# Kernel tuning notes

Hardware: AMD Instinct MI355X
Metric: run time of the kernel (lower is better)

## Reference

```python
import jax, jax.numpy as jnp
import numpy as np
import math

HEADS = 4
KV = 960
CH = (64, 128, 256, 512)
B, H, W = 8, 32, 32
EPS_IN = 1e-5  # nn.InstanceNorm2d default eps


def conv2d(x, w, groups=1, pad=0):
    # x: [N,C,H,W], w: [O, C//groups, kh, kw]
    return jax.lax.conv_general_dilated(
        x, w, (1, 1), [(pad, pad), (pad, pad)],
        feature_group_count=groups,
        dimension_numbers=('NCHW', 'OIHW', 'NCHW'))


def l2norm(x):
    # torch F.normalize(dim=-1): x / max(||x||_2, 1e-12)
    return x / jnp.maximum(jnp.linalg.norm(x, axis=-1, keepdims=True), 1e-12)


def setup_inputs() -> dict:
    key = jax.random.key(0)
    ks = iter(jax.random.split(key, 40))
    s = 0.02
    d = {}
    for i, c in enumerate(CH, 1):
        d[f'emb{i}'] = jax.random.normal(next(ks), (B, c, H, W), jnp.float32)
    d['emb_all'] = jax.random.normal(next(ks), (B, KV, H, W), jnp.float32)
    for i, c in enumerate(CH, 1):
        d[f'Wm{i}'] = jax.random.normal(next(ks), (c * HEADS, c, 1, 1), jnp.float32) * s
        # grouped 3x3: groups = c*HEADS//2 -> 2 in-channels per group
        d[f'Wq{i}'] = jax.random.normal(next(ks), (c * HEADS, 2, 3, 3), jnp.float32) * s
        d[f'Wp{i}'] = jax.random.normal(next(ks), (c, c, 1, 1), jnp.float32) * s
    d['Wmk'] = jax.random.normal(next(ks), (KV * HEADS, KV, 1, 1), jnp.float32) * s
    d['Wmv'] = jax.random.normal(next(ks), (KV * HEADS, KV, 1, 1), jnp.float32) * s
    # depthwise 3x3: groups = KV*HEADS
    d['Wk'] = jax.random.normal(next(ks), (KV * HEADS, 1, 3, 3), jnp.float32) * s
    d['Wv'] = jax.random.normal(next(ks), (KV * HEADS, 1, 3, 3), jnp.float32) * s
    return d


def _forward(emb1, emb2, emb3, emb4, emb_all,
             Wm1, Wq1, Wp1, Wm2, Wq2, Wp2, Wm3, Wq3, Wp3, Wm4, Wq4, Wp4,
             Wmk, Wmv, Wk, Wv):
    b, _, h, w = emb1.shape
    hw = h * w
    # shared K/V: 1x1 multi-head expand then depthwise 3x3
    k = conv2d(conv2d(emb_all, Wmk), Wk, groups=KV * HEADS, pad=1)
    v = conv2d(conv2d(emb_all, Wmv), Wv, groups=KV * HEADS, pad=1)
    k = l2norm(k.reshape(b, HEADS, KV, hw))   # [b,H,KV,hw]
    v = v.reshape(b, HEADS, KV, hw)
    scale = 1.0 / math.sqrt(KV)
    outs = []
    for emb, Wm, Wq, Wp in ((emb1, Wm1, Wq1, Wp1), (emb2, Wm2, Wq2, Wp2),
                            (emb3, Wm3, Wq3, Wp3), (emb4, Wm4, Wq4, Wp4)):
        c = emb.shape[1]
        q = conv2d(conv2d(emb, Wm), Wq, groups=c * HEADS // 2, pad=1)
        q = l2norm(q.reshape(b, HEADS, c, hw))            # [b,H,c,hw]
        attn = jnp.einsum('bhcn,bhdn->bhcd', q, k) * scale  # [b,H,c,KV]
        # InstanceNorm2d over (c, KV) per (b, head), no affine, biased var
        mu = attn.mean(axis=(2, 3), keepdims=True)
        var = attn.var(axis=(2, 3), keepdims=True)
        probs = jax.nn.softmax((attn - mu) / jnp.sqrt(var + EPS_IN), axis=-1)
        # dropout rate 0 (inference) -> identity
        out = jnp.einsum('bhcd,bhdn->bhcn', probs, v).mean(axis=1)  # head-mean -> [b,c,hw]
        outs.append(conv2d(out.reshape(b, c, h, w), Wp))
    return tuple(outs)


def reference(emb1, emb2, emb3, emb4, emb_all,
              Wm1, Wq1, Wp1, Wm2, Wq2, Wp2, Wm3, Wq3, Wp3, Wm4, Wq4, Wp4,
              Wmk, Wmv, Wk, Wv):
    return _forward(emb1, emb2, emb3, emb4, emb_all,
                    Wm1, Wq1, Wp1, Wm2, Wq2, Wp2, Wm3, Wq3, Wp3, Wm4, Wq4, Wp4,
                    Wmk, Wmv, Wk, Wv)
```

## Files before the change

kernel.cpp:

```cpp
#include <hip/hip_runtime.h>
#include <hip/hip_bf16.h>
#include <math.h>

typedef __hip_bfloat16 bf16;
typedef __attribute__((ext_vector_type(8))) short short8;
typedef __attribute__((ext_vector_type(8))) unsigned short u16x8;
typedef __attribute__((ext_vector_type(4))) float f32x4;
typedef long long ll;

#define B_ 8
#define HEADS_ 4
#define KV_ 960
#define HW_ 1024
#define CKV_ 3840

__device__ __forceinline__ float wredsum(float v) {
#pragma unroll
  for (int o = 32; o > 0; o >>= 1) v += __shfl_xor(v, o);
  return v;
}
__device__ __forceinline__ float wredmax(float v) {
#pragma unroll
  for (int o = 32; o > 0; o >>= 1) v = fmaxf(v, __shfl_xor(v, o));
  return v;
}

__device__ __forceinline__ float bfu2f(unsigned short u) {
  union { unsigned int i; float f; } c;
  c.i = ((unsigned int)u) << 16;
  return c.f;
}
__device__ __forceinline__ unsigned short f2bfu(float f) {
  bf16 h = __float2bfloat16(f);
  return *(unsigned short*)&h;
}

__device__ __forceinline__ void gl_lds16(const void* g, void* l) {
  __builtin_amdgcn_global_load_lds(
      (const __attribute__((address_space(1))) unsigned*)g,
      (__attribute__((address_space(3))) unsigned*)l, 16, 0, 0);
}

__global__ void __launch_bounds__(256) castw(const float* __restrict__ in,
                                             bf16* __restrict__ out, int n) {
  int i = (blockIdx.x * 256 + threadIdx.x) * 4;
  if (i < n) {
    float4 v = *(const float4*)(in + i);
    out[i] = __float2bfloat16(v.x);
    out[i + 1] = __float2bfloat16(v.y);
    out[i + 2] = __float2bfloat16(v.z);
    out[i + 3] = __float2bfloat16(v.w);
  }
}

template <typename InT>
__global__ void __launch_bounds__(256) tcast(const InT* __restrict__ in,
                                             bf16* __restrict__ out, int R,
                                             ll inZ, ll outZ) {
  __shared__ float t[32][33];
  const int x = threadIdx.x & 31, y0 = threadIdx.x >> 5;
  const int c0 = blockIdx.x << 5, r0 = blockIdx.y << 5;
  const InT* ip = in + (ll)blockIdx.z * inZ + (ll)r0 * 1024 + c0;
  bf16* op = out + (ll)blockIdx.z * outZ + (ll)c0 * R + r0;
#pragma unroll
  for (int i = 0; i < 4; i++) {
    int r = y0 + i * 8;
    float v;
    if constexpr (__is_same(InT, float)) v = ip[(ll)r * 1024 + x];
    else v = __bfloat162float(ip[(ll)r * 1024 + x]);
    t[r][x] = v;
  }
  __syncthreads();
#pragma unroll
  for (int i = 0; i < 4; i++) {
    int cc = y0 + i * 8;
    op[(ll)cc * R + x] = __float2bfloat16(t[x][cc]);
  }
}

template <int OUTMODE, bool STATS>
__global__ void __launch_bounds__(256) gemm_mfma(
    const bf16* __restrict__ A, const bf16* __restrict__ Bt, void* __restrict__ Y,
    int M, int N, int K, int nh,
    ll aZ, ll aH, ll bZ, ll bH, ll yZ, int ldy, float scale,
    float* __restrict__ part) {
  __shared__ bf16 As[2][128 * 32];
  __shared__ bf16 Bs[2][128 * 32];
  __shared__ float rs1[4], rs2[4];
  const int tid = threadIdx.x;
  const int lane = tid & 63;
  const int wave = tid >> 6;
  const int wr = wave >> 1, wc = wave & 1;

  const int gy = gridDim.y, gz = gridDim.z;
  int orig = (blockIdx.z * gy + blockIdx.y) * 8 + blockIdx.x;
  int cpx = (gy * gz);
  int flat = (orig & 7) * cpx + (orig >> 3);
  const int lx = flat & 7;
  int rest = flat >> 3;
  const int ly = rest % gy;
  const int lz = rest / gy;

  const int z = lz;
  const int m0 = ly << 7, n0 = lx << 7;

  f32x4 acc[4][4];
#pragma unroll
  for (int i = 0; i < 4; i++)
#pragma unroll
    for (int j = 0; j < 4; j++) acc[i][j] = (f32x4){0.f, 0.f, 0.f, 0.f};

  const int frow = lane & 15;
  const int kq = lane >> 4;

  const bf16* Ah = A + (ll)z * aZ;
  const bf16* Bh = Bt + (ll)z * bZ;
  int k0n = 0;

  auto stage = [&](int buf) {
#pragma unroll
    for (int t = 0; t < 2; t++) {
      const int e = (wave * 2 + t) * 64 + lane;
      const int row = e >> 2;
      const int ks = (e & 3) ^ ((row >> 1) & 3);
      int gr = m0 + row; gr = gr < M ? gr : M - 1;
      gl_lds16(Ah + (ll)gr * K + k0n + ks * 8,
               (char*)&As[buf][0] + (wave * 2 + t) * 1024);
      int rn = n0 + row; rn = rn < N ? rn : N - 1;
      gl_lds16(Bh + (ll)rn * K + k0n + ks * 8,
               (char*)&Bs[buf][0] + (wave * 2 + t) * 1024);
    }
  };

  const int kpt = K >> 5;
  const int iters = nh * kpt;
  stage(0);
  __syncthreads();

  int buf = 0;
  for (int it = 0; it < iters; ++it) {
    if (it + 1 < iters) {
      k0n += 32;
      if (k0n == K) { k0n = 0; Ah += aH; Bh += bH; }
      stage(buf ^ 1);
    }
    short8 af[4], bfr[4];
#pragma unroll
    for (int fm = 0; fm < 4; fm++) {
      const int row = wr * 64 + fm * 16 + frow;
      af[fm] = *(const short8*)&As[buf][((row << 2) | (kq ^ ((row >> 1) & 3))) << 3];
    }
#pragma unroll
    for (int fn = 0; fn < 4; fn++) {
      const int row = wc * 64 + fn * 16 + frow;
      bfr[fn] = *(const short8*)&Bs[buf][((row << 2) | (kq ^ ((row >> 1) & 3))) << 3];
    }
#pragma unroll
    for (int fm = 0; fm < 4; fm++)
#pragma unroll
      for (int fn = 0; fn < 4; fn++)
        acc[fm][fn] = __builtin_amdgcn_mfma_f32_16x16x32_bf16(
            af[fm], bfr[fn], acc[fm][fn], 0, 0, 0);
    __syncthreads();
    buf ^= 1;
  }

  const int rq = kq << 2;
  float lsum = 0.f, lsq = 0.f;
#pragma unroll
  for (int fm = 0; fm < 4; fm++) {
    const int mrow = m0 + wr * 64 + fm * 16 + rq;
#pragma unroll
    for (int fn = 0; fn < 4; fn++) {
      const int ncol = n0 + wc * 64 + fn * 16 + frow;
      if (ncol >= N) continue;
      if constexpr (OUTMODE == 0) {
        float* Yp = (float*)Y + (ll)z * yZ;
#pragma unroll
        for (int i = 0; i < 4; i++)
          if (mrow + i < M) {
            float v = acc[fm][fn][i] * scale;
            Yp[(ll)(mrow + i) * ldy + ncol] = v;
            if constexpr (STATS) { lsum += v; lsq += v * v; }
          }
      } else if constexpr (OUTMODE == 1) {
        bf16* Yp = (bf16*)Y + (ll)z * yZ;
#pragma unroll
        for (int i = 0; i < 4; i++)
          if (mrow + i < M)
            Yp[(ll)(mrow + i) * ldy + ncol] =
                __float2bfloat16(acc[fm][fn][i] * scale);
      } else {
        if (mrow < M) {
          bf16* Yp = (bf16*)Y + (ll)z * yZ + (ll)ncol * ldy + mrow;
#pragma unroll
          for (int i = 0; i < 4; i++)
            Yp[i] = __float2bfloat16(acc[fm][fn][i] * scale);
        }
      }
    }
  }
  if constexpr (STATS) {
    lsum = wredsum(lsum);
    lsq = wredsum(lsq);
    if (lane == 0) { rs1[wave] = lsum; rs2[wave] = lsq; }
    __syncthreads();
    if (tid == 0) {
      int slot = ly * 8 + lx;
      part[((ll)z * 32 + slot) * 2] = rs1[0] + rs1[1] + rs1[2] + rs1[3];
      part[((ll)z * 32 + slot) * 2 + 1] = rs2[0] + rs2[1] + rs2[2] + rs2[3];
    }
  }
}

template <int OUTMODE, bool STATS>
__global__ void __launch_bounds__(512, 2) gemm8(
    const bf16* __restrict__ A, const bf16* __restrict__ Bt, void* __restrict__ Y,
    int M, int N, int K, int nh,
    ll aZ, ll aH, ll bZ, ll bH, ll yZ, int ldy, float scale,
    float* __restrict__ part) {
  __shared__ char lds[131072];
  __shared__ float rs1[8], rs2[8];
  const int tid = threadIdx.x;
  const int lane = tid & 63;
  const int wave = tid >> 6;
  const int wm = wave >> 2, wn = wave & 3;

  const int nx = gridDim.x, my = gridDim.y;
  const int nwg = nx * my * gridDim.z;
  int orig = (blockIdx.z * my + blockIdx.y) * nx + blockIdx.x;
  int q8 = nwg >> 3, r8 = nwg & 7;
  int xcd = orig & 7, bidx = orig >> 3;
  int flat = (xcd < r8) ? xcd * (q8 + 1) + bidx
                        : r8 * (q8 + 1) + (xcd - r8) * q8 + bidx;
  const int lx = flat % nx;
  int rest = flat / nx;
  const int ly = rest % my;
  const int lz = rest / my;

  const int m0 = ly << 8, n0 = lx << 8;
  const int ktiles = K >> 6;
  const int nt = nh * ktiles;

  f32x4 acc[8][4];
#pragma unroll
  for (int i = 0; i < 8; i++)
#pragma unroll
    for (int j = 0; j < 4; j++) acc[i][j] = (f32x4){0.f, 0.f, 0.f, 0.f};

  const int frow = lane & 15;
  const int kq = lane >> 4;
  const int swz = frow & 7;

  auto stageRound = [&](int matB, int r, int tt, int buf) {
    int h = tt / ktiles;
    int koff = (tt % ktiles) << 6;
    int s = (r << 9) + tid;
    int row = s >> 3;
    int ks = (s & 7) ^ (row & 7);
    const bf16* src;
    char* dst;
    if (!matB) {
      int gr = m0 + row; gr = gr < M ? gr : M - 1;
      src = A + (ll)lz * aZ + (ll)h * aH + (ll)gr * K + koff + (ks << 3);
      dst = lds + buf * 32768 + (((r << 3) + wave) << 10);
    } else {
      int gr = n0 + row; gr = gr < N ? gr : N - 1;
      src = Bt + (ll)lz * bZ + (ll)h * bH + (ll)gr * K + koff + (ks << 3);
      dst = lds + 65536 + buf * 32768 + (((r << 3) + wave) << 10);
    }
    gl_lds16(src, dst);
  };

  auto readA = [&](int fm, int kh, int cur) -> short8 {
    int row = wm * 128 + fm * 16 + frow;
    int slot = (kq + (kh << 2)) ^ swz;
    return *(const short8*)(lds + cur * 32768 + row * 128 + slot * 16);
  };
  auto readB = [&](int fn, int kh, int cur) -> short8 {
    int row = wn * 64 + fn * 16 + frow;
    int slot = (kq + (kh << 2)) ^ swz;
    return *(const short8*)(lds + 65536 + cur * 32768 + row * 128 + slot * 16);
  };

  stageRound(1, 0, 0, 0); stageRound(1, 1, 0, 0);
  stageRound(1, 2, 0, 0); stageRound(1, 3, 0, 0);
  stageRound(0, 0, 0, 0); stageRound(0, 2, 0, 0);
  stageRound(0, 1, 0, 0); stageRound(0, 3, 0, 0);

  int cur = 0;
  for (int tt = 0; tt < nt; ++tt) {
    const bool hasNext = (tt + 1 < nt);
    short8 bfr[4][2];
#pragma unroll
    for (int p = 0; p < 4; p++) {
      if (p == 0) {
        if (hasNext) asm volatile("s_waitcnt vmcnt(2)" ::: "memory");
        else         asm volatile("s_waitcnt vmcnt(0)" ::: "memory");
        __builtin_amdgcn_s_barrier();
        __builtin_amdgcn_sched_barrier(0);
#pragma unroll
        for (int fn = 0; fn < 4; fn++)
#pragma unroll
          for (int kh = 0; kh < 2; kh++) bfr[fn][kh] = readB(fn, kh, cur);
      }
      if (p == 2) {
        if (hasNext) asm volatile("s_waitcnt vmcnt(6)" ::: "memory");
        __builtin_amdgcn_s_barrier();
        __builtin_amdgcn_sched_barrier(0);
      }
      short8 a0k0 = readA(2 * p, 0, cur), a0k1 = readA(2 * p, 1, cur);
      short8 a1k0 = readA(2 * p + 1, 0, cur), a1k1 = readA(2 * p + 1, 1, cur);
      if (hasNext) {
        if (p == 0) {
          stageRound(1, 0, tt + 1, cur ^ 1); stageRound(1, 1, tt + 1, cur ^ 1);
          stageRound(1, 2, tt + 1, cur ^ 1); stageRound(1, 3, tt + 1, cur ^ 1);
        } else if (p == 1) {
          stageRound(0, 0, tt + 1, cur ^ 1); stageRound(0, 2, tt + 1, cur ^ 1);
        } else if (p == 2) {
          stageRound(0, 1, tt + 1, cur ^ 1); stageRound(0, 3, tt + 1, cur ^ 1);
        }
      }
      __builtin_amdgcn_s_setprio(1);
#pragma unroll
      for (int fn = 0; fn < 4; fn++) {
        acc[2 * p][fn] = __builtin_amdgcn_mfma_f32_16x16x32_bf16(
            a0k0, bfr[fn][0], acc[2 * p][fn], 0, 0, 0);
        acc[2 * p][fn] = __builtin_amdgcn_mfma_f32_16x16x32_bf16(
            a0k1, bfr[fn][1], acc[2 * p][fn], 0, 0, 0);
        acc[2 * p + 1][fn] = __builtin_amdgcn_mfma_f32_16x16x32_bf16(
            a1k0, bfr[fn][0], acc[2 * p + 1][fn], 0, 0, 0);
        acc[2 * p + 1][fn] = __builtin_amdgcn_mfma_f32_16x16x32_bf16(
            a1k1, bfr[fn][1], acc[2 * p + 1][fn], 0, 0, 0);
      }
      __builtin_amdgcn_s_setprio(0);
    }
    cur ^= 1;
  }

  const int rq = kq << 2;
  float lsum = 0.f, lsq = 0.f;
#pragma unroll
  for (int fm = 0; fm < 8; fm++) {
    const int mrow = m0 + wm * 128 + fm * 16 + rq;
#pragma unroll
    for (int fn = 0; fn < 4; fn++) {
      const int ncol = n0 + wn * 64 + fn * 16 + frow;
      if (ncol >= N) continue;
      if constexpr (OUTMODE == 0) {
        float* Yp = (float*)Y + (ll)lz * yZ;
#pragma unroll
        for (int i = 0; i < 4; i++)
          if (mrow + i < M) {
            float v = acc[fm][fn][i] * scale;
            Yp[(ll)(mrow + i) * ldy + ncol] = v;
            if constexpr (STATS) { lsum += v; lsq += v * v; }
          }
      } else if constexpr (OUTMODE == 1) {
        bf16* Yp = (bf16*)Y + (ll)lz * yZ;
#pragma unroll
        for (int i = 0; i < 4; i++)
          if (mrow + i < M)
            Yp[(ll)(mrow + i) * ldy + ncol] =
                __float2bfloat16(acc[fm][fn][i] * scale);
      } else {
        if (mrow < M) {
          bf16* Yp = (bf16*)Y + (ll)lz * yZ + (ll)ncol * ldy + mrow;
#pragma unroll
          for (int i = 0; i < 4; i++)
            Yp[i] = __float2bfloat16(acc[fm][fn][i] * scale);
        }
      }
    }
  }
  if constexpr (STATS) {
    lsum = wredsum(lsum);
    lsq = wredsum(lsq);
    if (lane == 0) { rs1[wave] = lsum; rs2[wave] = lsq; }
    __syncthreads();
    if (tid == 0) {
      float s = 0.f, s2 = 0.f;
#pragma unroll
      for (int w = 0; w < 8; w++) { s += rs1[w]; s2 += rs2[w]; }
      int slot = ly * nx + lx;
      part[((ll)lz * 32 + slot) * 2] = s;
      part[((ll)lz * 32 + slot) * 2 + 1] = s2;
    }
  }
}

__global__ void __launch_bounds__(256) pv_reduce(const bf16* __restrict__ part,
                                                 bf16* __restrict__ out,
                                                 int planeShift) {
  const ll idx = ((ll)blockIdx.x * 256 + threadIdx.x) * 4;
  const int b = (int)(idx >> planeShift);
  const ll off = idx - ((ll)b << planeShift);
  const bf16* base = part + (((ll)b * 4) << planeShift) + off;
  float a0 = 0.f, a1 = 0.f, a2 = 0.f, a3 = 0.f;
#pragma unroll
  for (int s = 0; s < 4; s++) {
    ushort4 u = *(const ushort4*)(base + ((ll)s << planeShift));
    a0 += bfu2f(u.x); a1 += bfu2f(u.y); a2 += bfu2f(u.z); a3 += bfu2f(u.w);
  }
  ushort4 o;
  o.x = f2bfu(a0 * 0.25f);
  o.y = f2bfu(a1 * 0.25f);
  o.z = f2bfu(a2 * 0.25f);
  o.w = f2bfu(a3 * 0.25f);
  *(ushort4*)(out + idx) = o;
}

template <bool NORM>
__global__ void __launch_bounds__(256) dw3x3v(const bf16* __restrict__ in,
                                              const float* __restrict__ w9,
                                              bf16* __restrict__ out, int C) {
  __shared__ float tile[34][36];
  __shared__ float red[4];
  const int bc = blockIdx.x;
  const int ch = bc % C;
  const int tid = threadIdx.x;
  const int y = tid >> 3;
  const int x0 = (tid & 7) << 2;
  const bf16* ip = in + ((size_t)bc << 10);

  ushort4 u = *(const ushort4*)(ip + (y << 5) + x0);
  tile[y + 1][x0 + 1] = bfu2f(u.x);
  tile[y + 1][x0 + 2] = bfu2f(u.y);
  tile[y + 1][x0 + 3] = bfu2f(u.z);
  tile[y + 1][x0 + 4] = bfu2f(u.w);
  if (tid < 34) { tile[0][tid] = 0.f; tile[33][tid] = 0.f; }
  if (tid < 32) { tile[tid + 1][0] = 0.f; tile[tid + 1][33] = 0.f; }
  __syncthreads();

  const float* wc = w9 + ch * 9;
  float s[4] = {0.f, 0.f, 0.f, 0.f};
#pragma unroll
  for (int dy = 0; dy < 3; dy++) {
    const float* tr = &tile[y + dy][x0];
    float c0 = tr[0], c1 = tr[1], c2 = tr[2], c3 = tr[3], c4 = tr[4], c5 = tr[5];
    float wa = wc[dy * 3], wb = wc[dy * 3 + 1], wd = wc[dy * 3 + 2];
    s[0] += c0 * wa + c1 * wb + c2 * wd;
    s[1] += c1 * wa + c2 * wb + c3 * wd;
    s[2] += c2 * wa + c3 * wb + c4 * wd;
    s[3] += c3 * wa + c4 * wb + c5 * wd;
  }

  float inv = 1.f;
  if (NORM) {
    float ss = s[0] * s[0] + s[1] * s[1] + s[2] * s[2] + s[3] * s[3];
    ss = wredsum(ss);
    const int lane = tid & 63, wid = tid >> 6;
    if (lane == 0) red[wid] = ss;
    __syncthreads();
    inv = 1.0f / fmaxf(sqrtf(red[0] + red[1] + red[2] + red[3]), 1e-12f);
  }
  ushort4 o4;
  o4.x = f2bfu(s[0] * inv);
  o4.y = f2bfu(s[1] * inv);
  o4.z = f2bfu(s[2] * inv);
  o4.w = f2bfu(s[3] * inv);
  *(ushort4*)(out + ((size_t)bc << 10) + (y << 5) + x0) = o4;
}

__global__ void __launch_bounds__(256) dwtcast(const bf16* __restrict__ in,
                                               const float* __restrict__ w9,
                                               bf16* __restrict__ out) {
  __shared__ float t[3][32][34];
  const int jt = blockIdx.x;
  const int y = blockIdx.y;
  const int bh = blockIdx.z;
  const int b = bh >> 2, h = bh & 3;
  const int j0 = jt << 5;
  const int tid = threadIdx.x;

  if (tid < 192) {
    const int rr = tid / 64;
    const int rem = tid - rr * 64;
    const int jc = rem >> 1;
    const int half = rem & 1;
    const int iy = y - 1 + rr;
    float* dstp = &t[rr][jc][1 + (half << 4)];
    if (iy < 0 || iy > 31) {
#pragma unroll
      for (int u = 0; u < 16; u++) dstp[u] = 0.f;
    } else {
      const bf16* src = in + (((ll)b * CKV_ + h * KV_ + j0 + jc) << 10) +
                        (iy << 5) + (half << 4);
      u16x8 v0 = *(const u16x8*)src;
      u16x8 v1 = *(const u16x8*)(src + 8);
#pragma unroll
      for (int u = 0; u < 8; u++) dstp[u] = bfu2f(v0[u]);
#pragma unroll
      for (int u = 0; u < 8; u++) dstp[8 + u] = bfu2f(v1[u]);
    }
  }
  if (tid < 96) {
    const int rr = tid / 32, jc = tid - rr * 32;
    t[rr][jc][0] = 0.f;
    t[rr][jc][33] = 0.f;
  }
  __syncthreads();

  const int jp = tid & 15;
  const int xq = tid >> 4;
  const int ch0 = jp << 1;
  const float* wA = w9 + ((size_t)h * KV_ + j0 + ch0) * 9;
  const float* wB = wA + 9;

  bf16* orow = out + (ll)bh * 983040 + (ll)j0 + (ch0);
#pragma unroll
  for (int sx = 0; sx < 2; sx++) {
    const int x = xq + (sx << 4);
    float sA = 0.f, sB = 0.f;
#pragma unroll
    for (int dy = 0; dy < 3; dy++) {
      const float* rA = &t[dy][ch0][x];
      const float* rB = &t[dy][ch0 + 1][x];
      sA += rA[0] * wA[dy * 3] + rA[1] * wA[dy * 3 + 1] + rA[2] * wA[dy * 3 + 2];
      sB += rB[0] * wB[dy * 3] + rB[1] * wB[dy * 3 + 1] + rB[2] * wB[dy * 3 + 2];
    }
    const int n = (y << 5) + x;
    ushort2 o;
    o.x = f2bfu(sA);
    o.y = f2bfu(sB);
    *(ushort2*)(orow + (ll)n * 960) = o;
  }
}

__global__ void __launch_bounds__(256) gq3x3v(const bf16* __restrict__ in,
                                              const float* __restrict__ wq,
                                              bf16* __restrict__ out, int C4) {
  __shared__ float t0[34][36];
  __shared__ float t1[34][36];
  __shared__ float red[4];
  const int bo = blockIdx.x;
  const int o = bo % C4;
  const int b = bo / C4;
  const int ic0 = (o >> 1) << 1;
  const int tid = threadIdx.x;
  const int y = tid >> 3;
  const int x0 = (tid & 7) << 2;
  const bf16* p0 = in + (((size_t)b * C4 + ic0) << 10);

  ushort4 u0 = *(const ushort4*)(p0 + (y << 5) + x0);
  ushort4 u1 = *(const ushort4*)(p0 + 1024 + (y << 5) + x0);
  t0[y + 1][x0 + 1] = bfu2f(u0.x);
  t0[y + 1][x0 + 2] = bfu2f(u0.y);
  t0[y + 1][x0 + 3] = bfu2f(u0.z);
  t0[y + 1][x0 + 4] = bfu2f(u0.w);
  t1[y + 1][x0 + 1] = bfu2f(u1.x);
  t1[y + 1][x0 + 2] = bfu2f(u1.y);
  t1[y + 1][x0 + 3] = bfu2f(u1.z);
  t1[y + 1][x0 + 4] = bfu2f(u1.w);
  if (tid < 34) {
    t0[0][tid] = 0.f; t0[33][tid] = 0.f;
    t1[0][tid] = 0.f; t1[33][tid] = 0.f;
  }
  if (tid < 32) {
    t0[tid + 1][0] = 0.f; t0[tid + 1][33] = 0.f;
    t1[tid + 1][0] = 0.f; t1[tid + 1][33] = 0.f;
  }
  __syncthreads();

  const float* w = wq + o * 18;
  float s[4] = {0.f, 0.f, 0.f, 0.f};
#pragma unroll
  for (int dy = 0; dy < 3; dy++) {
    {
      const float* tr = &t0[y + dy][x0];
      float c0 = tr[0], c1 = tr[1], c2 = tr[2], c3 = tr[3], c4 = tr[4], c5 = tr[5];
      float wa = w[dy * 3], wb = w[dy * 3 + 1], wd = w[dy * 3 + 2];
      s[0] += c0 * wa + c1 * wb + c2 * wd;
      s[1] += c1 * wa + c2 * wb + c3 * wd;
      s[2] += c2 * wa + c3 * wb + c4 * wd;
      s[3] += c3 * wa + c4 * wb + c5 * wd;
    }
    {
      const float* tr = &t1[y + dy][x0];
      float c0 = tr[0], c1 = tr[1], c2 = tr[2], c3 = tr[3], c4 = tr[4], c5 = tr[5];
      float wa = w[9 + dy * 3], wb = w[9 + dy * 3 + 1], wd = w[9 + dy * 3 + 2];
      s[0] += c0 * wa + c1 * wb + c2 * wd;
      s[1] += c1 * wa + c2 * wb + c3 * wd;
      s[2] += c2 * wa + c3 * wb + c4 * wd;
      s[3] += c3 * wa + c4 * wb + c5 * wd;
    }
  }

  float ss = s[0] * s[0] + s[1] * s[1] + s[2] * s[2] + s[3] * s[3];
  ss = wredsum(ss);
  const int lane = tid & 63, wid = tid >> 6;
  if (lane == 0) red[wid] = ss;
  __syncthreads();
  float inv = 1.0f / fmaxf(sqrtf(red[0] + red[1] + red[2] + red[3]), 1e-12f);

  ushort4 o4;
  o4.x = f2bfu(s[0] * inv);
  o4.y = f2bfu(s[1] * inv);
  o4.z = f2bfu(s[2] * inv);
  o4.w = f2bfu(s[3] * inv);
  *(ushort4*)(out + ((size_t)bo << 10) + (y << 5) + x0) = o4;
}

__global__ void __launch_bounds__(256) softmax_rows(const float* __restrict__ attn,
                                                    const float* __restrict__ part,
                                                    int nslots,
                                                    bf16* __restrict__ probs, int c) {
  __shared__ float rm[4], rs[4];
  const int row = blockIdx.x;
  const int bh = row / c;
  const float* p = attn + (size_t)row * 960;
  bf16* op = probs + (size_t)row * 960;
  const int tid = threadIdx.x;

  float s = 0.f, s2 = 0.f;
  for (int i = 0; i < nslots; i++) {
    s += part[((ll)bh * 32 + i) * 2];
    s2 += part[((ll)bh * 32 + i) * 2 + 1];
  }
  const float n = (float)(c * 960);
  const float mu = s / n;
  const float var = s2 / n - mu * mu;
  const float rstd = rsqrtf(var + 1e-5f);

  float v[4];
  float mx = -1e30f;
#pragma unroll
  for (int u = 0; u < 4; u++) {
    int j = tid + (u << 8);
    if (j < 960) {
      v[u] = (p[j] - mu) * rstd;
      mx = fmaxf(mx, v[u]);
    } else {
      v[u] = -1e30f;
    }
  }
  mx = wredmax(mx);
  const int lane = tid & 63, wid = tid >> 6;
  if (lane == 0) rm[wid] = mx;
  __syncthreads();
  mx = fmaxf(fmaxf(rm[0], rm[1]), fmaxf(rm[2], rm[3]));

  float sum = 0.f;
#pragma unroll
  for (int u = 0; u < 4; u++) {
    int j = tid + (u << 8);
    if (j < 960) {
      v[u] = __expf(v[u] - mx);
      sum += v[u];
    }
  }
  sum = wredsum(sum);
  if (lane == 0) rs[wid] = sum;
  __syncthreads();
  sum = rs[0] + rs[1] + rs[2] + rs[3];
  const float inv = 1.0f / sum;
#pragma unroll
  for (int u = 0; u < 4; u++) {
    int j = tid + (u << 8);
    if (j < 960) op[j] = __float2bfloat16(v[u] * inv);
  }
}

static size_t p4_size(int nb) {
  const int chunkB = (nb + 1) / 2;
  size_t a = (size_t)nb * 4194304;
  size_t b = (size_t)nb * 1966080 + 7372800;
  size_t c = (size_t)chunkB * 7864320;
  size_t m = a > b ? a : b;
  return m > c ? m : c;
}
static size_t p5_size(int nb) {
  size_t a = (size_t)nb * 1048576;
  return a > 7372800 ? a : 7372800;
}
static size_t total_need(int nb) {
  return 3 * (size_t)nb * 7864320 + p4_size(nb) + p5_size(nb) + 3490816;
}

static void run_group(const float* const emb[4], const float* emb_all,
                      const float* const Wq[4],
                      const float* Wmk, const float* Wmv,
                      const float* Wk, const float* Wv,
                      bf16* Wm_all, bf16* Wp_all,
                      float* out, const size_t* out_off,
                      char* ws, int nb, hipStream_t stream) {
  const size_t szBig = (size_t)nb * 7864320;
  char* P1 = ws;
  char* P2 = P1 + szBig;
  char* P3 = P2 + szBig;
  char* P4 = P3 + szBig;
  char* P5 = P4 + p4_size(nb);
  char* FX = P5 + p5_size(nb);

  bf16* kbuf = (bf16*)P1;
  bf16* vt   = (bf16*)P2;
  bf16* kvexp = (bf16*)P3;
  float* attnb = (float*)P3;
  bf16* pvpart = (bf16*)P3;
  bf16* embT_all = (bf16*)P4;
  bf16* Wmv_bf = (bf16*)(P4 + (size_t)nb * 1966080);
  bf16* qbuf = (bf16*)P4;
  bf16* probsb = (bf16*)P4;
  bf16* Wmk_bf = (bf16*)P5;
  bf16* OtT = (bf16*)P5;
  float* part = (float*)(FX + 3482112);

  const float qk_scale = 1.0f / sqrtf((float)KV_);
  const int CHs[4] = {64, 128, 256, 512};
  const size_t wm_off[4] = {0, 16384, 81920, 344064};
  const size_t wp_off[4] = {0, 4096, 20480, 86016};

  castw<<<3600, 256, 0, stream>>>(Wmk, Wmk_bf, 3686400);
  castw<<<3600, 256, 0, stream>>>(Wmv, Wmv_bf, 3686400);
  tcast<float><<<dim3(32, 30, nb), 256, 0, stream>>>(emb_all, embT_all, 960,
                                                     983040LL, 983040LL);
  gemm8<1, false><<<dim3(4, 15, nb), 512, 0, stream>>>(
      Wmk_bf, embT_all, kvexp, 3840, 1024, 960, 1, 0, 0, 983040LL, 0,
      3932160LL, 1024, 1.f, nullptr);
  dw3x3v<true><<<nb * CKV_, 256, 0, stream>>>(kvexp, Wk, kbuf, CKV_);
  gemm8<1, false><<<dim3(4, 15, nb), 512, 0, stream>>>(
      Wmv_bf, embT_all, kvexp, 3840, 1024, 960, 1, 0, 0, 983040LL, 0,
      3932160LL, 1024, 1.f, nullptr);
  dwtcast<<<dim3(30, 32, nb * 4), 256, 0, stream>>>(kvexp, Wv, vt);

  for (int br = 0; br < 4; br++) {
    const int c = CHs[br];
    const int C4 = c * 4;
    const int mtiles = (c + 127) / 128;
    bf16* Wm_bf = Wm_all + wm_off[br];
    bf16* Wp_bf = Wp_all + wp_off[br];
    int planeShift = 10;
    for (int t = c; t > 1; t >>= 1) planeShift++;

    tcast<float><<<dim3(32, c / 32, nb), 256, 0, stream>>>(
        emb[br], qbuf, c, (ll)c * 1024, (ll)c * 1024);
    if (c == 512) {
      gemm8<1, false><<<dim3(4, C4 / 256, nb), 512, 0, stream>>>(
          Wm_bf, qbuf, kvexp, C4, 1024, c, 1, 0, 0, (ll)c * 1024, 0,
          (ll)C4 * 1024, 1024, 1.f, nullptr);
    } else {
      gemm_mfma<1, false><<<dim3(8, C4 / 128, nb), 256, 0, stream>>>(
          Wm_bf, qbuf, kvexp, C4, 1024, c, 1, 0, 0, (ll)c * 1024, 0,
          (ll)C4 * 1024, 1024, 1.f, nullptr);
    }
    gq3x3v<<<nb * C4, 256, 0, stream>>>(kvexp, Wq[br], qbuf, C4);
    int nslots;
    if (c == 512) {
      gemm8<0, true><<<dim3(4, c / 256, nb * 4), 512, 0, stream>>>(
          qbuf, kbuf, attnb, c, 960, 1024, 1, (ll)c * 1024, 0, 983040LL, 0,
          (ll)c * 960, 960, qk_scale, part);
      nslots = (c / 256) * 4;
    } else {
      gemm_mfma<0, true><<<dim3(8, mtiles, nb * 4), 256, 0, stream>>>(
          qbuf, kbuf, attnb, c, 960, 1024, 1, (ll)c * 1024, 0, 983040LL, 0,
          (ll)c * 960, 960, qk_scale, part);
      nslots = mtiles * 8;
    }
    softmax_rows<<<nb * 4 * c, 256, 0, stream>>>(attnb, part, nslots, probsb, c);
    if (c == 512) {
      gemm8<2, false><<<dim3(4, c / 256, nb * 4), 512, 0, stream>>>(
          probsb, vt, pvpart, c, 1024, 960, 1, (ll)c * 960, 0, 983040LL, 0,
          (ll)1024 * c, c, 1.f, nullptr);
    } else {
      gemm_mfma<2, false><<<dim3(8, mtiles, nb * 4), 256, 0, stream>>>(
          probsb, vt, pvpart, c, 1024, 960, 1, (ll)c * 960, 0, 983040LL, 0,
          (ll)1024 * c, c, 1.f, nullptr);
    }
    pv_reduce<<<nb * c, 256, 0, stream>>>(pvpart, OtT, planeShift);
    gemm_mfma<0, false><<<dim3(8, mtiles, nb), 256, 0, stream>>>(
        Wp_bf, OtT, out + out_off[br], c, 1024, c, 1, 0, 0,
        (ll)1024 * c, 0, (ll)c * 1024, 1024, 1.f, nullptr);
  }
}

extern "C" void kernel_launch(void* const* d_in, const int* in_sizes, int n_in,
                              void* d_out, int out_size, void* d_ws, size_t ws_size,
                              hipStream_t stream) {
  const float* emb[4] = {(const float*)d_in[0], (const float*)d_in[1],
                         (const float*)d_in[2], (const float*)d_in[3]};
  const float* emb_all = (const float*)d_in[4];
  const float* Wm[4] = {(const float*)d_in[5], (const float*)d_in[8],
                        (const float*)d_in[11], (const float*)d_in[14]};
  const float* Wq[4] = {(const float*)d_in[6], (const float*)d_in[9],
                        (const float*)d_in[12], (const float*)d_in[15]};
  const float* Wp[4] = {(const float*)d_in[7], (const float*)d_in[10],
                        (const float*)d_in[13], (const float*)d_in[16]};
  const float* Wmk = (const float*)d_in[17];
  const float* Wmv = (const float*)d_in[18];
  const float* Wk = (const float*)d_in[19];
  const float* Wv = (const float*)d_in[20];
  float* out = (float*)d_out;

  const int CHs[4] = {64, 128, 256, 512};
  const size_t out_off_full[4] = {0, 524288, 1572864, 3670016};
  const size_t wm_off[4] = {0, 16384, 81920, 344064};
  const size_t wp_off[4] = {0, 4096, 20480, 86016};

  int nb = 1;
  if (ws_size >= total_need(8)) nb = 8;
  else if (ws_size >= total_need(4)) nb = 4;
  else if (ws_size >= total_need(2)) nb = 2;

  char* FX = (char*)d_ws + 3 * (size_t)nb * 7864320 + p4_size(nb) + p5_size(nb);
  bf16* Wm_all = (bf16*)FX;
  bf16* Wp_all = (bf16*)(FX + 2785280);

  for (int br = 0; br < 4; br++) {
    const int c = CHs[br];
    castw<<<(4 * c * c / 4 + 255) / 256, 256, 0, stream>>>(
        Wm[br], Wm_all + wm_off[br], 4 * c * c);
    castw<<<(c * c / 4 + 255) / 256, 256, 0, stream>>>(
        Wp[br], Wp_all + wp_off[br], c * c);
  }

  for (int b0 = 0; b0 < B_; b0 += nb) {
    const float* embB[4];
    for (int i = 0; i < 4; i++) embB[i] = emb[i] + (size_t)b0 * CHs[i] * HW_;
    const float* emb_allB = emb_all + (size_t)b0 * KV_ * HW_;
    size_t out_offB[4];
    for (int i = 0; i < 4; i++)
      out_offB[i] = out_off_full[i] + (size_t)b0 * CHs[i] * HW_;
    run_group(embB, emb_allB, Wq, Wmk, Wmv, Wk, Wv, Wm_all, Wp_all,
              out, out_offB, (char*)d_ws, nb, stream);
  }
}
```

Measured before the change: 806.7 us.

## Store attention scores as bf16, vectorize softmax, compute both group outputs per conv block

After: 752.2 us, median of 2. 1.07x faster.

```diff
diff --git a/kernel.cpp b/kernel.cpp
--- a/kernel.cpp
+++ b/kernel.cpp
@@ -187,9 +187,11 @@
         bf16* Yp = (bf16*)Y + (ll)z * yZ;
 #pragma unroll
         for (int i = 0; i < 4; i++)
-          if (mrow + i < M)
-            Yp[(ll)(mrow + i) * ldy + ncol] =
-                __float2bfloat16(acc[fm][fn][i] * scale);
+          if (mrow + i < M) {
+            float v = acc[fm][fn][i] * scale;
+            Yp[(ll)(mrow + i) * ldy + ncol] = __float2bfloat16(v);
+            if constexpr (STATS) { lsum += v; lsq += v * v; }
+          }
       } else {
         if (mrow < M) {
           bf16* Yp = (bf16*)Y + (ll)z * yZ + (ll)ncol * ldy + mrow;
@@ -360,9 +362,11 @@
         bf16* Yp = (bf16*)Y + (ll)lz * yZ;
 #pragma unroll
         for (int i = 0; i < 4; i++)
-          if (mrow + i < M)
-            Yp[(ll)(mrow + i) * ldy + ncol] =
-                __float2bfloat16(acc[fm][fn][i] * scale);
+          if (mrow + i < M) {
+            float v = acc[fm][fn][i] * scale;
+            Yp[(ll)(mrow + i) * ldy + ncol] = __float2bfloat16(v);
+            if constexpr (STATS) { lsum += v; lsq += v * v; }
+          }
       } else {
         if (mrow < M) {
           bf16* Yp = (bf16*)Y + (ll)lz * yZ + (ll)ncol * ldy + mrow;
@@ -527,16 +531,17 @@
   }
 }
 
-__global__ void __launch_bounds__(256) gq3x3v(const bf16* __restrict__ in,
-                                              const float* __restrict__ wq,
-                                              bf16* __restrict__ out, int C4) {
+__global__ void __launch_bounds__(256) gq3x3v2(const bf16* __restrict__ in,
+                                               const float* __restrict__ wq,
+                                               bf16* __restrict__ out, int C4) {
   __shared__ float t0[34][36];
   __shared__ float t1[34][36];
-  __shared__ float red[4];
+  __shared__ float red[8];
+  const int G = C4 >> 1;
   const int bo = blockIdx.x;
-  const int o = bo % C4;
-  const int b = bo / C4;
-  const int ic0 = (o >> 1) << 1;
+  const int g = bo % G;
+  const int b = bo / G;
+  const int ic0 = g << 1;
   const int tid = threadIdx.x;
   const int y = tid >> 3;
   const int x0 = (tid & 7) << 2;
@@ -562,55 +567,71 @@
   }
   __syncthreads();
 
-  const float* w = wq + o * 18;
-  float s[4] = {0.f, 0.f, 0.f, 0.f};
+  const float* wA = wq + (size_t)(ic0) * 18;
+  const float* wB = wq + (size_t)(ic0 + 1) * 18;
+  float sA[4] = {0.f, 0.f, 0.f, 0.f};
+  float sB[4] = {0.f, 0.f, 0.f, 0.f};
 #pragma unroll
   for (int dy = 0; dy < 3; dy++) {
+    const float* r0 = &t0[y + dy][x0];
+    const float* r1 = &t1[y + dy][x0];
+    float c0 = r0[0], c1 = r0[1], c2 = r0[2], c3 = r0[3], c4 = r0[4], c5 = r0[5];
+    float d0 = r1[0], d1 = r1[1], d2 = r1[2], d3 = r1[3], d4 = r1[4], d5 = r1[5];
     {
-      const float* tr = &t0[y + dy][x0];
-      float c0 = tr[0], c1 = tr[1], c2 = tr[2], c3 = tr[3], c4 = tr[4], c5 = tr[5];
-      float wa = w[dy * 3], wb = w[dy * 3 + 1], wd = w[dy * 3 + 2];
-      s[0] += c0 * wa + c1 * wb + c2 * wd;
-      s[1] += c1 * wa + c2 * wb + c3 * wd;
-      s[2] += c2 * wa + c3 * wb + c4 * wd;
-      s[3] += c3 * wa + c4 * wb + c5 * wd;
+      float wa = wA[dy * 3], wb = wA[dy * 3 + 1], wd = wA[dy * 3 + 2];
+      float va = wA[9 + dy * 3], vb = wA[9 + dy * 3 + 1], vd = wA[9 + dy * 3 + 2];
+      sA[0] += c0 * wa + c1 * wb + c2 * wd + d0 * va + d1 * vb + d2 * vd;
+      sA[1] += c1 * wa + c2 * wb + c3 * wd + d1 * va + d2 * vb + d3 * vd;
+      sA[2] += c2 * wa + c3 * wb + c4 * wd + d2 * va + d3 * vb + d4 * vd;
+      sA[3] += c3 * wa + c4 * wb + c5 * wd + d3 * va + d4 * vb + d5 * vd;
     }
     {
-      const float* tr = &t1[y + dy][x0];
-      float c0 = tr[0], c1 = tr[1], c2 = tr[2], c3 = tr[3], c4 = tr[4], c5 = tr[5];
-      float wa = w[9 + dy * 3], wb = w[9 + dy * 3 + 1], wd = w[9 + dy * 3 + 2];
-      s[0] += c0 * wa + c1 * wb + c2 * wd;
-      s[1] += c1 * wa + c2 * wb + c3 * wd;
-      s[2] += c2 * wa + c3 * wb + c4 * wd;
-      s[3] += c3 * wa + c4 * wb + c5 * wd;
-    }
-  }
-
-  float ss = s[0] * s[0] + s[1] * s[1] + s[2] * s[2] + s[3] * s[3];
-  ss = wredsum(ss);
+      float wa = wB[dy * 3], wb = wB[dy * 3 + 1], wd = wB[dy * 3 + 2];
+      float va = wB[9 + dy * 3], vb = wB[9 + dy * 3 + 1], vd = wB[9 + dy * 3 + 2];
+      sB[0] += c0 * wa + c1 * wb + c2 * wd + d0 * va + d1 * vb + d2 * vd;
+      sB[1] += c1 * wa + c2 * wb + c3 * wd + d1 * va + d2 * vb + d3 * vd;
+      sB[2] += c2 * wa + c3 * wb + c4 * wd + d2 * va + d3 * vb + d4 * vd;
+      sB[3] += c3 * wa + c4 * wb + c5 * wd + d3 * va + d4 * vb + d5 * vd;
+    }
+  }
+
+  float ssA = sA[0] * sA[0] + sA[1] * sA[1] + sA[2] * sA[2] + sA[3] * sA[3];
+  float ssB = sB[0] * sB[0] + sB[1] * sB[1] + sB[2] * sB[2] + sB[3] * sB[3];
+  ssA = wredsum(ssA);
+  ssB = wredsum(ssB);
   const int lane = tid & 63, wid = tid >> 6;
-  if (lane == 0) red[wid] = ss;
+  if (lane == 0) { red[wid * 2] = ssA; red[wid * 2 + 1] = ssB; }
   __syncthreads();
-  float inv = 1.0f / fmaxf(sqrtf(red[0] + red[1] + red[2] + red[3]), 1e-12f);
-
-  ushort4 o4;
-  o4.x = f2bfu(s[0] * inv);
-  o4.y = f2bfu(s[1] * inv);
-  o4.z = f2bfu(s[2] * inv);
-  o4.w = f2bfu(s[3] * inv);
-  *(ushort4*)(out + ((size_t)bo << 10) + (y << 5) + x0) = o4;
-}
-
-__global__ void __launch_bounds__(256) softmax_rows(const float* __restrict__ attn,
+  float invA = 1.0f / fmaxf(sqrtf(red[0] + red[2] + red[4] + red[6]), 1e-12f);
+  float invB = 1.0f / fmaxf(sqrtf(red[1] + red[3] + red[5] + red[7]), 1e-12f);
+
+  bf16* opA = out + (((size_t)b * C4 + ic0) << 10) + (y << 5) + x0;
+  ushort4 oA;
+  oA.x = f2bfu(sA[0] * invA);
+  oA.y = f2bfu(sA[1] * invA);
+  oA.z = f2bfu(sA[2] * invA);
+  oA.w = f2bfu(sA[3] * invA);
+  *(ushort4*)opA = oA;
+  ushort4 oB;
+  oB.x = f2bfu(sB[0] * invB);
+  oB.y = f2bfu(sB[1] * invB);
+  oB.z = f2bfu(sB[2] * invB);
+  oB.w = f2bfu(sB[3] * invB);
+  *(ushort4*)(opA + 1024) = oB;
+}
+
+__global__ void __launch_bounds__(256) softmax_rows(const bf16* __restrict__ attn,
                                                     const float* __restrict__ part,
                                                     int nslots,
                                                     bf16* __restrict__ probs, int c) {
   __shared__ float rm[4], rs[4];
   const int row = blockIdx.x;
   const int bh = row / c;
-  const float* p = attn + (size_t)row * 960;
+  const bf16* p = attn + (size_t)row * 960;
   bf16* op = probs + (size_t)row * 960;
   const int tid = threadIdx.x;
+  const int j0 = tid << 2;
+  const bool act = (j0 < 960);
 
   float s = 0.f, s2 = 0.f;
   for (int i = 0; i < nslots; i++) {
@@ -624,15 +645,13 @@
 
   float v[4];
   float mx = -1e30f;
-#pragma unroll
-  for (int u = 0; u < 4; u++) {
-    int j = tid + (u << 8);
-    if (j < 960) {
-      v[u] = (p[j] - mu) * rstd;
-      mx = fmaxf(mx, v[u]);
-    } else {
-      v[u] = -1e30f;
-    }
+  if (act) {
+    ushort4 u = *(const ushort4*)(p + j0);
+    v[0] = (bfu2f(u.x) - mu) * rstd;
+    v[1] = (bfu2f(u.y) - mu) * rstd;
+    v[2] = (bfu2f(u.z) - mu) * rstd;
+    v[3] = (bfu2f(u.w) - mu) * rstd;
+    mx = fmaxf(fmaxf(v[0], v[1]), fmaxf(v[2], v[3]));
   }
   mx = wredmax(mx);
   const int lane = tid & 63, wid = tid >> 6;
@@ -641,10 +660,9 @@
   mx = fmaxf(fmaxf(rm[0], rm[1]), fmaxf(rm[2], rm[3]));
 
   float sum = 0.f;
-#pragma unroll
-  for (int u = 0; u < 4; u++) {
-    int j = tid + (u << 8);
-    if (j < 960) {
+  if (act) {
+#pragma unroll
+    for (int u = 0; u < 4; u++) {
       v[u] = __expf(v[u] - mx);
       sum += v[u];
     }
@@ -654,10 +672,13 @@
   __syncthreads();
   sum = rs[0] + rs[1] + rs[2] + rs[3];
   const float inv = 1.0f / sum;
-#pragma unroll
-  for (int u = 0; u < 4; u++) {
-    int j = tid + (u << 8);
-    if (j < 960) op[j] = __float2bfloat16(v[u] * inv);
+  if (act) {
+    ushort4 o;
+    o.x = f2bfu(v[0] * inv);
+    o.y = f2bfu(v[1] * inv);
+    o.z = f2bfu(v[2] * inv);
+    o.w = f2bfu(v[3] * inv);
+    *(ushort4*)(op + j0) = o;
   }
 }
 
@@ -695,7 +716,7 @@
   bf16* kbuf = (bf16*)P1;
   bf16* vt   = (bf16*)P2;
   bf16* kvexp = (bf16*)P3;
-  float* attnb = (float*)P3;
+  bf16* attnb = (bf16*)P3;
   bf16* pvpart = (bf16*)P3;
   bf16* embT_all = (bf16*)P4;
   bf16* Wmv_bf = (bf16*)(P4 + (size_t)nb * 1966080);
@@ -743,15 +764,15 @@
           Wm_bf, qbuf, kvexp, C4, 1024, c, 1, 0, 0, (ll)c * 1024, 0,
           (ll)C4 * 1024, 1024, 1.f, nullptr);
     }
-    gq3x3v<<<nb * C4, 256, 0, stream>>>(kvexp, Wq[br], qbuf, C4);
+    gq3x3v2<<<nb * (C4 / 2), 256, 0, stream>>>(kvexp, Wq[br], qbuf, C4);
     int nslots;
     if (c == 512) {
-      gemm8<0, true><<<dim3(4, c / 256, nb * 4), 512, 0, stream>>>(
+      gemm8<1, true><<<dim3(4, c / 256, nb * 4), 512, 0, stream>>>(
           qbuf, kbuf, attnb, c, 960, 1024, 1, (ll)c * 1024, 0, 983040LL, 0,
           (ll)c * 960, 960, qk_scale, part);
       nslots = (c / 256) * 4;
     } else {
-      gemm_mfma<0, true><<<dim3(8, mtiles, nb * 4), 256, 0, stream>>>(
+      gemm_mfma<1, true><<<dim3(8, mtiles, nb * 4), 256, 0, stream>>>(
           qbuf, kbuf, attnb, c, 960, 1024, 1, (ll)c * 1024, 0, 983040LL, 0,
           (ll)c * 960, 960, qk_scale, part);
       nslots = mtiles * 8;
```
